# Performance work log

Measured on AMD Instinct MI355X. Metric: run time of the kernel, lower is better.

## Reference

```python
import jax, jax.numpy as jnp
import numpy as np

LEAKY_SLOPE = 0.01

def bilinear_interpolate(grid, coords):
    # grid: [H, W, C]; coords: [N, 2] in [0,1] (x, y order as in torch code)
    H = grid.shape[0] - 1
    W = grid.shape[1] - 1
    fx = coords[:, 0] * W
    fy = coords[:, 1] * H
    x0 = fx.astype(jnp.int32)
    y0 = fy.astype(jnp.int32)
    xf = jnp.mod(fx, 1.0)
    yf = jnp.mod(fy, 1.0)
    x1 = jnp.minimum(x0 + 1, W)
    y1 = jnp.minimum(y0 + 1, H)
    tl = grid[y0, x0]  # [N, C]
    tr = grid[y0, x1]
    bl = grid[y1, x0]
    br = grid[y1, x1]
    xf = xf[:, None]
    yf = yf[:, None]
    top = (1.0 - xf) * tl + xf * tr
    bot = (1.0 - xf) * bl + xf * br
    return (1.0 - yf) * top + yf * bot


def setup_inputs() -> dict:
    key = jax.random.key(0)
    ks = jax.random.split(key, 10)
    N = 2097152
    pos = jax.random.uniform(ks[0], (N, 2), dtype=jnp.float32)
    dir = jax.random.uniform(ks[1], (N, 2), dtype=jnp.float32)
    pos_grid = jax.random.normal(ks[2], (256, 256, 3), dtype=jnp.float32) * 10.0
    dir_grid = jax.random.normal(ks[3], (256, 256, 3), dtype=jnp.float32) * 10.0
    # Linear layers: PyTorch default init U(-1/sqrt(fan_in), 1/sqrt(fan_in))
    def linear(kw, kb, fan_in, fan_out):
        bound = 1.0 / np.sqrt(fan_in)
        W = jax.random.uniform(kw, (fan_out, fan_in), minval=-bound, maxval=bound, dtype=jnp.float32)
        b = jax.random.uniform(kb, (fan_out,), minval=-bound, maxval=bound, dtype=jnp.float32)
        return W, b
    W1, b1 = linear(ks[4], ks[5], 6, 64)
    W2, b2 = linear(ks[6], ks[7], 64, 64)
    W3, b3 = linear(ks[8], ks[9], 64, 1)
    return {"pos": pos, "dir": dir, "pos_grid": pos_grid, "dir_grid": dir_grid,
            "W1": W1, "b1": b1, "W2": W2, "b2": b2, "W3": W3, "b3": b3}


def reference(pos, dir, pos_grid, dir_grid, W1, b1, W2, b2, W3, b3):
    pos_feat = jax.lax.stop_gradient(bilinear_interpolate(pos_grid, pos))  # .detach() in torch
    dir_feat = jax.lax.stop_gradient(bilinear_interpolate(dir_grid, dir))
    x = jnp.concatenate([pos_feat, dir_feat], axis=1)  # [N, 6]
    x = jax.nn.leaky_relu(x @ W1.T + b1, LEAKY_SLOPE)
    x = jax.nn.leaky_relu(x @ W2.T + b2, LEAKY_SLOPE)
    return jax.nn.sigmoid(x @ W3.T + b3)  # [N, 1]
```

## Files before the change

kernel.cpp:

```cpp
#include <hip/hip_runtime.h>
#include <hip/hip_bf16.h>
#include <math.h>


#define NTHREADS 256
#define NB 4

typedef __attribute__((ext_vector_type(4))) short s16x4;
typedef __attribute__((ext_vector_type(4))) float f32x4;
typedef __attribute__((ext_vector_type(4))) int i32x4;
typedef __attribute__((ext_vector_type(2))) int i32x2;

static __device__ __forceinline__ short f2bf(float f) {
    return __builtin_bit_cast(short, __float2bfloat16(f));
}
static __device__ __forceinline__ int pk2(float lo, float hi) {
    unsigned short l = (unsigned short)f2bf(lo);
    unsigned short h = (unsigned short)f2bf(hi);
    return (int)(((unsigned int)h << 16) | (unsigned int)l);
}
static __device__ __forceinline__ float bflo(int u) {
    return __builtin_bit_cast(float, u << 16);
}
static __device__ __forceinline__ float bfhi(int u) {
    return __builtin_bit_cast(float, (int)(u & 0xffff0000));
}

__global__ __launch_bounds__(256) void make_patches(
    const float* __restrict__ gP, const float* __restrict__ gD,
    int* __restrict__ outP, int* __restrict__ outD) {
    int gid = blockIdx.x * 256 + threadIdx.x;
    const float* g = (gid < 65536) ? gP : gD;
    int* po = (gid < 65536) ? outP : outD;
    int id = gid & 65535;
    int y0 = id >> 8, x0 = id & 255;
    int x1 = min(x0 + 1, 255), y1 = min(y0 + 1, 255);
    const float* tl = g + (y0 * 256 + x0) * 3;
    const float* tr = g + (y0 * 256 + x1) * 3;
    const float* bl = g + (y1 * 256 + x0) * 3;
    const float* br = g + (y1 * 256 + x1) * 3;
    i32x4 u0;
    i32x2 u1;
    u0[0] = pk2(tl[0], bl[0]);
    u0[1] = pk2(tl[1], bl[1]);
    u0[2] = pk2(tl[2], bl[2]);
    u0[3] = pk2(tr[0], br[0]);
    u1[0] = pk2(tr[1], br[1]);
    u1[1] = pk2(tr[2], br[2]);
    *(i32x4*)(po + id * 8) = u0;
    *(i32x2*)(po + id * 8 + 4) = u1;
}

static __device__ __forceinline__ void patch_issue(
    const int* __restrict__ tab, float px, float py, int* P, float& xf,
    float& yf) {
    float fx = px * 255.0f;
    float fy = py * 255.0f;
    int x0 = (int)fx;
    int y0 = (int)fy;
    xf = fx - floorf(fx);
    yf = fy - floorf(fy);
    int idx = (y0 << 8) | x0;
    i32x4 a = *(const i32x4*)(tab + idx * 8);
    i32x2 b = *(const i32x2*)(tab + idx * 8 + 4);
    P[0] = a[0]; P[1] = a[1]; P[2] = a[2];
    P[3] = a[3]; P[4] = b[0]; P[5] = b[1];
}

static __device__ __forceinline__ void patch_lerp(const int* P, float xf,
                                                  float yf, float* f) {
#pragma unroll
    for (int ch = 0; ch < 3; ++ch) {
        float tl = bflo(P[ch]), bl = bfhi(P[ch]);
        float tr = bflo(P[ch + 3]), br = bfhi(P[ch + 3]);
        float top = fmaf(xf, tr - tl, tl);
        float bot = fmaf(xf, br - bl, bl);
        f[ch] = fmaf(yf, bot - top, top);
    }
}

__global__ __launch_bounds__(NTHREADS, 3) void mlp_mfma_kernel(
    const float* __restrict__ pos, const float* __restrict__ dir,
    const int* __restrict__ patP, const int* __restrict__ patD,
    const float* __restrict__ W1, const float* __restrict__ b1,
    const float* __restrict__ W2, const float* __restrict__ b2,
    const float* __restrict__ W3, const float* __restrict__ b3,
    float* __restrict__ out) {
    __shared__ int lds_F[4 * 2 * 64 * 4];

    const int w = threadIdx.x >> 6;
    const int lane = threadIdx.x & 63;
    const int c = lane & 15;
    const int q = lane >> 4;

    int* FB = lds_F + w * (2 * 64 * 4);

    s16x4 A1f[4];
#pragma unroll
    for (int mt = 0; mt < 4; ++mt) {
        int f = mt * 16 + c;
        s16x4 t;
#pragma unroll
        for (int j = 0; j < 4; ++j) {
            int k = q * 4 + j;
            float v = 0.0f;
            if (k < 6) v = W1[f * 6 + k];
            else if (k == 6) v = b1[f];
            t[j] = f2bf(v);
        }
        A1f[mt] = t;
    }
    s16x4 A2f[4][4];
#pragma unroll
    for (int kt = 0; kt < 4; ++kt)
#pragma unroll
        for (int mt = 0; mt < 4; ++mt) {
            int n2 = mt * 16 + c;
            int k0 = kt * 16 + q * 4;
            s16x4 t;
#pragma unroll
            for (int j = 0; j < 4; ++j) t[j] = f2bf(W2[n2 * 64 + k0 + j]);
            A2f[kt][mt] = t;
        }
    f32x4 ci[4], w3q[4];
#pragma unroll
    for (int mt = 0; mt < 4; ++mt)
#pragma unroll
        for (int r = 0; r < 4; ++r) {
            ci[mt][r] = b2[mt * 16 + q * 4 + r];
            w3q[mt][r] = W3[mt * 16 + q * 4 + r];
        }
    const float b3s = b3[0];
    const int dbias = pk2(1.0f, 0.0f);
    const f32x4 zacc = {0.f, 0.f, 0.f, 0.f};

    const long wave_global = (long)blockIdx.x * 4 + w;
    const long base0 = wave_global * (64L * NB);
    const float2* pos2 = (const float2*)pos;
    const float2* dir2 = (const float2*)dir;

    float2 cp1, cd1;
    {
        float2 c0p = pos2[base0 + lane], c0d = dir2[base0 + lane];
        cp1 = pos2[base0 + 64 + lane];
        cd1 = dir2[base0 + 64 + lane];
        int P0_[12];
        float fr0[4];
        patch_issue(patP, c0p.x, c0p.y, P0_, fr0[0], fr0[1]);
        patch_issue(patD, c0d.x, c0d.y, P0_ + 6, fr0[2], fr0[3]);
        float feat[6];
        patch_lerp(P0_, fr0[0], fr0[1], feat);
        patch_lerp(P0_ + 6, fr0[2], fr0[3], feat + 3);
        i32x4 dv;
        dv[0] = pk2(feat[0], feat[1]);
        dv[1] = pk2(feat[2], feat[3]);
        dv[2] = pk2(feat[4], feat[5]);
        dv[3] = dbias;
        *(i32x4*)(FB + lane * 4) = dv;
    }

#pragma unroll 1
    for (int ib = 0; ib < NB; ++ib) {
        const long base = base0 + ib * 64;
        const int cur = ib & 1;

        int PB[12];
        float frB[4];
        patch_issue(patP, cp1.x, cp1.y, PB, frB[0], frB[1]);
        patch_issue(patD, cd1.x, cd1.y, PB + 6, frB[2], frB[3]);

        {
            int mb = min(ib + 2, NB - 1);
            cp1 = pos2[base0 + mb * 64 + lane];
            cd1 = dir2[base0 + mb * 64 + lane];
        }

        float s[4];
#pragma unroll
        for (int t = 0; t < 4; ++t) {
            i32x2 bi = *(const i32x2*)(FB + cur * 256 + (t * 16 + c) * 4 +
                                       (q & 1) * 2);
            s16x4 bfeat = __builtin_bit_cast(s16x4, bi);

            f32x4 a1[4];
#pragma unroll
            for (int mt = 0; mt < 4; ++mt)
                a1[mt] = __builtin_amdgcn_mfma_f32_16x16x16bf16_1k(
                    A1f[mt], bfeat, zacc, 0, 0, 0);

            s16x4 bh[4];
#pragma unroll
            for (int kt = 0; kt < 4; ++kt) {
                s16x4 hv;
#pragma unroll
                for (int r = 0; r < 4; ++r) {
                    float x = a1[kt][r];
                    hv[r] = f2bf(fmaxf(x, 0.01f * x));
                }
                bh[kt] = hv;
            }

            f32x4 a2[4];
#pragma unroll
            for (int mt = 0; mt < 4; ++mt) a2[mt] = ci[mt];
#pragma unroll
            for (int kt = 0; kt < 4; ++kt)
#pragma unroll
                for (int mt = 0; mt < 4; ++mt)
                    a2[mt] = __builtin_amdgcn_mfma_f32_16x16x16bf16_1k(
                        A2f[kt][mt], bh[kt], a2[mt], 0, 0, 0);

            float tt = 0.0f;
#pragma unroll
            for (int mt = 0; mt < 4; ++mt)
#pragma unroll
                for (int r = 0; r < 4; ++r) {
                    float x = a2[mt][r];
                    x = fmaxf(x, 0.01f * x);
                    tt = fmaf(x, w3q[mt][r], tt);
                }
            tt += __shfl_xor(tt, 16, 64);
            tt += __shfl_xor(tt, 32, 64);
            s[t] = tt;
        }

        float sa = (q & 1) ? s[1] : s[0];
        float sb = (q & 1) ? s[3] : s[2];
        float v = (q & 2) ? sb : sa;
        v += b3s;
        v = 1.0f / (1.0f + __expf(-v));
        out[base + q * 16 + c] = v;

        {
            float feat[6];
            patch_lerp(PB, frB[0], frB[1], feat);
            patch_lerp(PB + 6, frB[2], frB[3], feat + 3);
            i32x4 dv;
            dv[0] = pk2(feat[0], feat[1]);
            dv[1] = pk2(feat[2], feat[3]);
            dv[2] = pk2(feat[4], feat[5]);
            dv[3] = dbias;
            *(i32x4*)(FB + (cur ^ 1) * 256 + lane * 4) = dv;
        }
    }
}

extern "C" void kernel_launch(void* const* d_in, const int* in_sizes, int n_in,
                              void* d_out, int out_size, void* d_ws,
                              size_t ws_size, hipStream_t stream) {
    const float* pos = (const float*)d_in[0];
    const float* dir = (const float*)d_in[1];
    const float* pos_grid = (const float*)d_in[2];
    const float* dir_grid = (const float*)d_in[3];
    const float* W1 = (const float*)d_in[4];
    const float* b1 = (const float*)d_in[5];
    const float* W2 = (const float*)d_in[6];
    const float* b2 = (const float*)d_in[7];
    const float* W3 = (const float*)d_in[8];
    const float* b3 = (const float*)d_in[9];
    float* out = (float*)d_out;

    int* patP = (int*)d_ws;
    int* patD = patP + 65536 * 8;

    make_patches<<<512, 256, 0, stream>>>(pos_grid, dir_grid, patP, patD);

    const int n = in_sizes[0] / 2;
    const int batches = n / 64;
    const int waves = batches / NB;
    const int blocks = waves / 4;

    mlp_mfma_kernel<<<blocks, NTHREADS, 0, stream>>>(
        pos, dir, patP, patD, W1, b1, W2, b2, W3, b3, out);
}
```

Baseline: 155.8 us.

## Switch MLP to 16x16x32 bf16 MFMA with register-permute operand exchange

Replaces the 16x16x16 bf16 MFMAs with the gfx950 16x16x32 variant, which halves the MFMA count for layer 2 and folds layer 1 into K=32 with mostly zero padding. The LDS staging buffer for features is removed. Features and hidden activations are now redistributed between lanes with ds_bpermute, and the software pipeline is reordered so the current batch's lerp happens at the top of the loop. This trades LDS writes and reads plus fewer MFMA issues for extra bpermute traffic, and the lane mapping of the permutes could be wrong.

Result: slower. 158.9 us (+2.0%).

```diff
diff --git a/kernel.cpp b/kernel.cpp
--- a/kernel.cpp
+++ b/kernel.cpp
@@ -6,7 +6,7 @@
 #define NTHREADS 256
 #define NB 4
 
-typedef __attribute__((ext_vector_type(4))) short s16x4;
+typedef __attribute__((ext_vector_type(8))) short bf16x8;
 typedef __attribute__((ext_vector_type(4))) float f32x4;
 typedef __attribute__((ext_vector_type(4))) int i32x4;
 typedef __attribute__((ext_vector_type(2))) int i32x2;
@@ -24,6 +24,12 @@
 }
 static __device__ __forceinline__ float bfhi(int u) {
     return __builtin_bit_cast(float, (int)(u & 0xffff0000));
+}
+static __device__ __forceinline__ int selperm(int addr, int pa, int pb,
+                                              bool hi) {
+    int va = __builtin_amdgcn_ds_bpermute(addr, pa);
+    int vb = __builtin_amdgcn_ds_bpermute(addr, pb);
+    return hi ? vb : va;
 }
 
 __global__ __launch_bounds__(256) void make_patches(
@@ -86,40 +92,36 @@
     const float* __restrict__ W2, const float* __restrict__ b2,
     const float* __restrict__ W3, const float* __restrict__ b3,
     float* __restrict__ out) {
-    __shared__ int lds_F[4 * 2 * 64 * 4];
-
-    const int w = threadIdx.x >> 6;
     const int lane = threadIdx.x & 63;
     const int c = lane & 15;
     const int q = lane >> 4;
 
-    int* FB = lds_F + w * (2 * 64 * 4);
-
-    s16x4 A1f[4];
+    bf16x8 A1f[4];
 #pragma unroll
     for (int mt = 0; mt < 4; ++mt) {
         int f = mt * 16 + c;
-        s16x4 t;
-#pragma unroll
-        for (int j = 0; j < 4; ++j) {
-            int k = q * 4 + j;
+        bf16x8 t;
+#pragma unroll
+        for (int j = 0; j < 8; ++j) {
             float v = 0.0f;
-            if (k < 6) v = W1[f * 6 + k];
-            else if (k == 6) v = b1[f];
+            if (q == 0) {
+                if (j < 6) v = W1[f * 6 + j];
+                else if (j == 6) v = b1[f];
+            }
             t[j] = f2bf(v);
         }
         A1f[mt] = t;
     }
-    s16x4 A2f[4][4];
-#pragma unroll
-    for (int kt = 0; kt < 4; ++kt)
+    bf16x8 A2f[2][4];
+#pragma unroll
+    for (int kt = 0; kt < 2; ++kt)
 #pragma unroll
         for (int mt = 0; mt < 4; ++mt) {
             int n2 = mt * 16 + c;
-            int k0 = kt * 16 + q * 4;
-            s16x4 t;
-#pragma unroll
-            for (int j = 0; j < 4; ++j) t[j] = f2bf(W2[n2 * 64 + k0 + j]);
+            int k0 = kt * 32 + q * 8;
+            bf16x8 t;
+#pragma unroll
+            for (int j = 0; j < 8; ++j) t[j] = f2bf(W2[n2 * 64 + k0 + j]);
             A2f[kt][mt] = t;
         }
     f32x4 ci[4], w3q[4];
@@ -134,41 +136,42 @@
     const int dbias = pk2(1.0f, 0.0f);
     const f32x4 zacc = {0.f, 0.f, 0.f, 0.f};
 
-    const long wave_global = (long)blockIdx.x * 4 + w;
+    const int exA = ((((q & 1) * 2) * 16) + c) * 4;
+    const int exB = exA + 64;
+    const bool hi = (q >= 2);
+
+    const long wave_global = (long)(blockIdx.x * 4) + (threadIdx.x >> 6);
     const long base0 = wave_global * (64L * NB);
     const float2* pos2 = (const float2*)pos;
     const float2* dir2 = (const float2*)dir;
 
+    int PA[12];
+    float frA[4];
     float2 cp1, cd1;
     {
         float2 c0p = pos2[base0 + lane], c0d = dir2[base0 + lane];
         cp1 = pos2[base0 + 64 + lane];
         cd1 = dir2[base0 + 64 + lane];
-        int P0_[12];
-        float fr0[4];
-        patch_issue(patP, c0p.x, c0p.y, P0_, fr0[0], fr0[1]);
-        patch_issue(patD, c0d.x, c0d.y, P0_ + 6, fr0[2], fr0[3]);
-        float feat[6];
-        patch_lerp(P0_, fr0[0], fr0[1], feat);
-        patch_lerp(P0_ + 6, fr0[2], fr0[3], feat + 3);
-        i32x4 dv;
-        dv[0] = pk2(feat[0], feat[1]);
-        dv[1] = pk2(feat[2], feat[3]);
-        dv[2] = pk2(feat[4], feat[5]);
-        dv[3] = dbias;
-        *(i32x4*)(FB + lane * 4) = dv;
+        patch_issue(patP, c0p.x, c0p.y, PA, frA[0], frA[1]);
+        patch_issue(patD, c0d.x, c0d.y, PA + 6, frA[2], frA[3]);
     }
 
 #pragma unroll 1
     for (int ib = 0; ib < NB; ++ib) {
         const long base = base0 + ib * 64;
-        const int cur = ib & 1;
-
-        int PB[12];
-        float frB[4];
-        patch_issue(patP, cp1.x, cp1.y, PB, frB[0], frB[1]);
-        patch_issue(patD, cd1.x, cd1.y, PB + 6, frB[2], frB[3]);
-
+
+        int d0, d1, d2;
+        {
+            float feat[6];
+            patch_lerp(PA, frA[0], frA[1], feat);
+            patch_lerp(PA + 6, frA[2], frA[3], feat + 3);
+            d0 = pk2(feat[0], feat[1]);
+            d1 = pk2(feat[2], feat[3]);
+            d2 = pk2(feat[4], feat[5]);
+        }
+
+        patch_issue(patP, cp1.x, cp1.y, PA, frA[0], frA[1]);
+        patch_issue(patD, cd1.x, cd1.y, PA + 6, frA[2], frA[3]);
         {
             int mb = min(ib + 2, NB - 1);
             cp1 = pos2[base0 + mb * 64 + lane];
@@ -177,38 +180,47 @@
 
         float s[4];
 #pragma unroll
-        for (int t = 0; t < 4; ++t) {
-            i32x2 bi = *(const i32x2*)(FB + cur * 256 + (t * 16 + c) * 4 +
-                                       (q & 1) * 2);
-            s16x4 bfeat = __builtin_bit_cast(s16x4, bi);
+        for (int pt = 0; pt < 4; ++pt) {
+            const int fa = (pt * 16 + c) * 4;
+            i32x4 bi;
+            bi[0] = __builtin_amdgcn_ds_bpermute(fa, d0);
+            bi[1] = __builtin_amdgcn_ds_bpermute(fa, d1);
+            bi[2] = __builtin_amdgcn_ds_bpermute(fa, d2);
+            bi[3] = dbias;
+            bf16x8 bfeat = __builtin_bit_cast(bf16x8, bi);
 
             f32x4 a1[4];
 #pragma unroll
             for (int mt = 0; mt < 4; ++mt)
-                a1[mt] = __builtin_amdgcn_mfma_f32_16x16x16bf16_1k(
+                a1[mt] = __builtin_amdgcn_mfma_f32_16x16x32_bf16(
                     A1f[mt], bfeat, zacc, 0, 0, 0);
 
-            s16x4 bh[4];
-#pragma unroll
-            for (int kt = 0; kt < 4; ++kt) {
-                s16x4 hv;
-#pragma unroll
-                for (int r = 0; r < 4; ++r) {
-                    float x = a1[kt][r];
-                    hv[r] = f2bf(fmaxf(x, 0.01f * x));
+            int Pk[4][2];
+#pragma unroll
+            for (int mt = 0; mt < 4; ++mt) {
+#pragma unroll
+                for (int rr = 0; rr < 2; ++rr) {
+                    float x0 = a1[mt][2 * rr], x1 = a1[mt][2 * rr + 1];
+                    x0 = fmaxf(x0, 0.01f * x0);
+                    x1 = fmaxf(x1, 0.01f * x1);
+                    Pk[mt][rr] = pk2(x0, x1);
                 }
-                bh[kt] = hv;
             }
 
             f32x4 a2[4];
 #pragma unroll
-            for (int mt = 0; mt < 4; ++mt) a2[mt] = ci[mt];
-#pragma unroll
-            for (int kt = 0; kt < 4; ++kt)
+            for (int kt = 0; kt < 2; ++kt) {
+                i32x4 Q;
+                Q[0] = selperm(exA, Pk[2 * kt][0], Pk[2 * kt + 1][0], hi);
+                Q[1] = selperm(exA, Pk[2 * kt][1], Pk[2 * kt + 1][1], hi);
+                Q[2] = selperm(exB, Pk[2 * kt][0], Pk[2 * kt + 1][0], hi);
+                Q[3] = selperm(exB, Pk[2 * kt][1], Pk[2 * kt + 1][1], hi);
+                bf16x8 bq = __builtin_bit_cast(bf16x8, Q);
 #pragma unroll
                 for (int mt = 0; mt < 4; ++mt)
-                    a2[mt] = __builtin_amdgcn_mfma_f32_16x16x16bf16_1k(
-                        A2f[kt][mt], bh[kt], a2[mt], 0, 0, 0);
+                    a2[mt] = __builtin_amdgcn_mfma_f32_16x16x32_bf16(
+                        A2f[kt][mt], bq, kt == 0 ? ci[mt] : a2[mt], 0, 0, 0);
+            }
 
             float tt = 0.0f;
 #pragma unroll
@@ -221,7 +233,7 @@
                 }
             tt += __shfl_xor(tt, 16, 64);
             tt += __shfl_xor(tt, 32, 64);
-            s[t] = tt;
+            s[pt] = tt;
         }
 
         float sa = (q & 1) ? s[1] : s[0];
@@ -230,18 +242,6 @@
         v += b3s;
         v = 1.0f / (1.0f + __expf(-v));
         out[base + q * 16 + c] = v;
-
-        {
-            float feat[6];
-            patch_lerp(PB, frB[0], frB[1], feat);
-            patch_lerp(PB + 6, frB[2], frB[3], feat + 3);
-            i32x4 dv;
-            dv[0] = pk2(feat[0], feat[1]);
-            dv[1] = pk2(feat[2], feat[3]);
-            dv[2] = pk2(feat[4], feat[5]);
-            dv[3] = dbias;
-            *(i32x4*)(FB + (cur ^ 1) * 256 + lane * 4) = dv;
-        }
     }
 }
 
```
